# Kernel optimization log

Measured on AMD Instinct MI355X. Metric: run time of the kernel, lower is better.

Reference implementation:

```python
import jax, jax.numpy as jnp
import numpy as np

B, C, H, W = 2, 256, 128, 128
S = 256          # num superpixels
QK = 256         # qk_dim
NUM_HEADS = 8
TOPK = 128
SCALE = (QK // NUM_HEADS) ** -0.5
EPS = 1e-5


def setup_inputs() -> dict:
    key = jax.random.key(0)
    k0, k1, k2, k3, k4 = jax.random.split(key, 5)
    x = jax.random.normal(k0, (B, C, H, W), jnp.float32)
    affinity_matrix = jax.random.normal(k1, (B, S, H * W), jnp.float32)
    wq = jax.random.normal(k2, (QK, C), jnp.float32) * 0.05
    wk = jax.random.normal(k3, (QK, C), jnp.float32) * 0.05
    wv = jax.random.normal(k4, (C, C), jnp.float32) * 0.05
    return {
        "x": x,
        "affinity_matrix": affinity_matrix,
        "ln_weight": jnp.ones((C,), jnp.float32),
        "ln_bias": jnp.zeros((C,), jnp.float32),
        "wq": wq,
        "wk": wk,
        "wv": wv,
        "num_spixels": S,
    }


def _forward(x, affinity_matrix, ln_weight, ln_bias, wq, wk, wv, num_spixels):
    Bx, Cx, Hx, Wx = x.shape
    HW = Hx * Wx
    h = NUM_HEADS
    T = TOPK
    Sx = num_spixels

    # LayerNorm2d: normalize over channel dim per pixel
    mu = x.mean(axis=1, keepdims=True)
    var = ((x - mu) ** 2).mean(axis=1, keepdims=True)
    xn = (x - mu) * jax.lax.rsqrt(var + EPS)
    xn = xn * ln_weight[None, :, None, None] + ln_bias[None, :, None, None]
    xf = xn.reshape(Bx, Cx, HW)

    # 1x1 convs as GEMMs: [out_ch, in_ch] x [B, in_ch, HW]
    q = jnp.einsum('oc,bcn->bon', wq, xf)   # [B, QK, HW]
    k = jnp.einsum('oc,bcn->bon', wk, xf)   # [B, QK, HW]
    v = jnp.einsum('oc,bcn->bon', wv, xf)   # [B, C,  HW]

    # top-k pixels per superpixel
    sims, indices = jax.lax.top_k(affinity_matrix, T)  # [B, S, T]

    def gath(t):  # t [B, D, HW] -> [B, D, S, T]
        return jax.vmap(lambda tb, ib: tb[:, ib])(t, indices)

    def heads(t):  # [B, D, S, T] -> [B, S, h, T, D//h]
        D = t.shape[1]
        return t.reshape(Bx, h, D // h, Sx, T).transpose(0, 3, 1, 4, 2)

    qh = heads(gath(q))  # [B,S,h,T,cq]
    kh = heads(gath(k))
    vh = heads(gath(v))  # [B,S,h,T,cv]

    attn = jnp.einsum('bshtc,bshuc->bshtu', qh, kh) * SCALE
    attn = jax.nn.softmax(attn, axis=-1)

    w = sims[:, :, None, :, None]            # [B,S,1,T,1]
    vw = vh * w                               # kweight=True
    out = jnp.einsum('bshtu,bshuc->bshtc', attn, vw)

    # 'b k h t c -> b (h c) (k t)'
    out = out.transpose(0, 2, 4, 1, 3).reshape(Bx, Cx, Sx * T)
    out = out * sims.reshape(Bx, 1, Sx * T)  # weight is broadcast over channels

    idx = indices.reshape(Bx, Sx * T)
    # weighted_scatter_mean with normz=False: tgt is v itself (not zeros)
    res = jax.vmap(lambda vb, ib, sb: vb.at[:, ib].add(sb))(v, idx, out)
    return res.reshape(Bx, Cx, Hx, Wx)


def reference(x, affinity_matrix, ln_weight, ln_bias, wq, wk, wv, num_spixels):
    return _forward(x, affinity_matrix, ln_weight, ln_bias, wq, wk, wv, num_spixels)
```

## Files before the change

### kernel.cpp

```cpp
#include <hip/hip_runtime.h>

#define HW      16384
#define C_DIM   256
#define S_DIM   256
#define T_K     128
#define NH      8
#define DH      32
#define QKV_ST  768
#define B_DIM   2
#define SCALE_F 0.17677669529663687f
#define CAND    1536
#define EQCAP   512
#define NROWS   (S_DIM * T_K)

typedef __attribute__((ext_vector_type(8))) short short8;
typedef __attribute__((ext_vector_type(4))) float f32x4;
typedef __attribute__((ext_vector_type(4))) unsigned uint4v;

__device__ __forceinline__ short f2bf(float f) {
    union { __bf16 h; short s; } u;
    u.h = (__bf16)f;
    return u.s;
}
__device__ __forceinline__ float bf2f(short s) {
    unsigned u = ((unsigned)(unsigned short)s) << 16;
    return __uint_as_float(u);
}

__device__ __forceinline__ unsigned sortkey(float f) {
    unsigned u = __float_as_uint(f);
    return (u & 0x80000000u) ? ~u : (u | 0x80000000u);
}
__device__ __forceinline__ float keyval(unsigned k) {
    return __uint_as_float((k & 0x80000000u) ? (k ^ 0x80000000u) : ~k);
}

__launch_bounds__(256)
__global__ void ln_fused_kernel(const float* __restrict__ x,
                                const float* __restrict__ g,
                                const float* __restrict__ beta,
                                short* __restrict__ xnT) {
    int b  = blockIdx.y;
    int n0 = blockIdx.x * 64;
    int tid = threadIdx.x;

    __shared__ float t[256][67];
    __shared__ float ps[4][64], pss[4][64];
    __shared__ float mu_s[64], rs_s[64];

    {
        int cl = tid >> 2;
        int ni = (tid & 3) * 16;
#pragma unroll
        for (int gset = 0; gset < 4; gset++) {
            int c = cl + gset * 64;
            const float* src = x + ((size_t)b * C_DIM + c) * HW + n0 + ni;
#pragma unroll
            for (int j = 0; j < 4; j++) {
                float4 v = *(const float4*)(src + j * 4);
                t[c][ni + j * 4 + 0] = v.x;
                t[c][ni + j * 4 + 1] = v.y;
                t[c][ni + j * 4 + 2] = v.z;
                t[c][ni + j * 4 + 3] = v.w;
            }
        }
    }
    __syncthreads();

    {
        int q = tid >> 6;
        int l = tid & 63;
        float s = 0.f, ss = 0.f;
#pragma unroll
        for (int c = 0; c < 64; c++) {
            float v = t[q * 64 + c][l];
            s += v; ss += v * v;
        }
        ps[q][l] = s; pss[q][l] = ss;
    }
    __syncthreads();
    if (tid < 64) {
        float S  = ps[0][tid] + ps[1][tid] + ps[2][tid] + ps[3][tid];
        float SS = pss[0][tid] + pss[1][tid] + pss[2][tid] + pss[3][tid];
        float m   = S * (1.f / C_DIM);
        float var = fmaxf(SS * (1.f / C_DIM) - m * m, 0.f);
        mu_s[tid] = m;
        rs_s[tid] = rsqrtf(var + 1e-5f);
    }
    __syncthreads();

    {
        int nl  = tid >> 2;
        int ci0 = (tid & 3) * 16;
        float m  = mu_s[nl];
        float rs = rs_s[nl];
        short* dst = xnT + ((size_t)b * HW + n0 + nl) * C_DIM;
#pragma unroll
        for (int gset = 0; gset < 4; gset++) {
            int ci = ci0 + gset * 64;
            short8 s0, s1;
#pragma unroll
            for (int j = 0; j < 8; j++) {
                int c = ci + j;
                s0[j] = f2bf((t[c][nl] - m) * rs * g[c] + beta[c]);
            }
#pragma unroll
            for (int j = 0; j < 8; j++) {
                int c = ci + 8 + j;
                s1[j] = f2bf((t[c][nl] - m) * rs * g[c] + beta[c]);
            }
            *(short8*)(dst + ci)     = s0;
            *(short8*)(dst + ci + 8) = s1;
        }
    }
}

__global__ void wpack_kernel(const float* __restrict__ wq,
                             const float* __restrict__ wk,
                             const float* __restrict__ wv,
                             short* __restrict__ wb) {
    int gid  = blockIdx.x * 256 + threadIdx.x;
    int base = gid * 4;
    int o = base >> 8;
    int c = base & 255;
    const float* src = (o < 256) ? wq + (size_t)o * 256
                     : (o < 512) ? wk + (size_t)(o - 256) * 256
                                 : wv + (size_t)(o - 512) * 256;
    float4 w4 = *(const float4*)(src + c);
    short4 s4;
    s4.x = f2bf(w4.x); s4.y = f2bf(w4.y); s4.z = f2bf(w4.z); s4.w = f2bf(w4.w);
    *(short4*)&wb[base] = s4;
}

#define E_STRIDE 136
#define A_STR   36
__launch_bounds__(256)
__global__ void qkv_mfma_kernel(const short* __restrict__ xnT,
                                const short* __restrict__ wb,
                                short* __restrict__ qkv) {
    int b  = blockIdx.z;
    int n0 = blockIdx.x * 128;
    int o0 = blockIdx.y * 128;
    int tid  = threadIdx.x;
    int wv   = tid >> 6;
    int wn   = wv & 1;
    int wo   = wv >> 1;
    int lane = tid & 63;
    int quad = lane >> 4;
    int ln   = lane & 15;

    __shared__ __align__(16) union {
        short S[2][128 * A_STR];
        short Es[64 * E_STRIDE];
    } L;

    int r1 = tid >> 2,        q1 = tid & 3;
    int r2 = (tid + 256) >> 2, q2 = (tid + 256) & 3;
    const short* gA1 = xnT + ((size_t)b * HW + n0 + r1) * C_DIM + q1 * 8;
    const short* gA2 = xnT + ((size_t)b * HW + n0 + r2) * C_DIM + q2 * 8;
    const short* gB1 = wb + (size_t)(o0 + r1) * C_DIM + q1 * 8;
    const short* gB2 = wb + (size_t)(o0 + r2) * C_DIM + q2 * 8;
    int la1 = r1 * A_STR + q1 * 8;
    int la2 = r2 * A_STR + q2 * 8;

    int aoff[4], boff[4];
#pragma unroll
    for (int mt = 0; mt < 4; mt++)
        aoff[mt] = (wn * 64 + mt * 16 + ln) * A_STR + quad * 8;
#pragma unroll
    for (int nt = 0; nt < 4; nt++)
        boff[nt] = (wo * 64 + nt * 16 + ln) * A_STR + quad * 8;

    f32x4 acc[4][4];
    const f32x4 zero4 = {0.f, 0.f, 0.f, 0.f};
#pragma unroll
    for (int mt = 0; mt < 4; mt++)
#pragma unroll
        for (int nt = 0; nt < 4; nt++) acc[mt][nt] = zero4;

    {
        short8 ra1 = *(const short8*)gA1;
        short8 ra2 = *(const short8*)gA2;
        short8 rb1 = *(const short8*)gB1;
        short8 rb2 = *(const short8*)gB2;
        *(short8*)&L.S[0][la1] = ra1;
        *(short8*)&L.S[0][la2] = ra2;
        *(short8*)&L.S[1][la1] = rb1;
        *(short8*)&L.S[1][la2] = rb2;
    }
    __syncthreads();

    for (int t = 0; t < 8; t++) {
        short8 ra1, ra2, rb1, rb2;
        if (t < 7) {
            int c0 = (t + 1) * 32;
            ra1 = *(const short8*)(gA1 + c0);
            ra2 = *(const short8*)(gA2 + c0);
            rb1 = *(const short8*)(gB1 + c0);
            rb2 = *(const short8*)(gB2 + c0);
        }

        short8 af[4], bf[4];
#pragma unroll
        for (int mt = 0; mt < 4; mt++) af[mt] = *(const short8*)&L.S[0][aoff[mt]];
#pragma unroll
        for (int nt = 0; nt < 4; nt++) bf[nt] = *(const short8*)&L.S[1][boff[nt]];
        __builtin_amdgcn_s_setprio(1);
#pragma unroll
        for (int mt = 0; mt < 4; mt++)
#pragma unroll
            for (int nt = 0; nt < 4; nt++)
                acc[mt][nt] = __builtin_amdgcn_mfma_f32_16x16x32_bf16(af[mt], bf[nt], acc[mt][nt], 0, 0, 0);
        __builtin_amdgcn_s_setprio(0);

        __syncthreads();
        if (t < 7) {
            *(short8*)&L.S[0][la1] = ra1;
            *(short8*)&L.S[0][la2] = ra2;
            *(short8*)&L.S[1][la1] = rb1;
            *(short8*)&L.S[1][la2] = rb2;
            __syncthreads();
        }
    }

#pragma unroll
    for (int p = 0; p < 2; p++) {
        if (wn == p) {
#pragma unroll
            for (int mt = 0; mt < 4; mt++)
#pragma unroll
                for (int nt = 0; nt < 4; nt++)
#pragma unroll
                    for (int r = 0; r < 4; r++)
                        L.Es[(mt * 16 + quad * 4 + r) * E_STRIDE + wo * 64 + nt * 16 + ln] =
                            f2bf(acc[mt][nt][r]);
        }
        __syncthreads();
        {
            int nl = tid >> 2;
            int qo = (tid & 3) * 32;
            const short* srcr = &L.Es[nl * E_STRIDE + qo];
            short* dst = qkv + ((size_t)b * HW + n0 + p * 64 + nl) * QKV_ST + o0 + qo;
#pragma unroll
            for (int j = 0; j < 4; j++)
                *(short8*)(dst + j * 8) = *(const short8*)(srcr + j * 8);
        }
        __syncthreads();
    }
}

__launch_bounds__(1024)
__global__ void topk_kernel(const float* __restrict__ aff,
                            float* __restrict__ sims,
                            int* __restrict__ idx,
                            int* __restrict__ cnt) {
    int s = blockIdx.x, b = blockIdx.y;
    int tid = threadIdx.x;
    const float4* rowv4 = (const float4*)(aff + ((size_t)b * S_DIM + s) * HW);
    int* cntb = cnt + b * HW;

    __shared__ union {
        unsigned rowk[HW];
        unsigned short eqix_u[EQCAP];
    } U;
    __shared__ unsigned hist[256];
    __shared__ unsigned sufs[256];
    __shared__ unsigned ckey[CAND];
    __shared__ unsigned short cidx[CAND];
    __shared__ int s_sel, cHi, cCand, cEq;

    if (tid == 0) { cHi = 0; cCand = 0; cEq = 0; }
    if (tid < 256) hist[tid] = 0;
    __syncthreads();

    for (int i = tid; i < HW / 4; i += 1024) {
        float4 v = rowv4[i];
        uint4v k;
        k[0] = sortkey(v.x); k[1] = sortkey(v.y);
        k[2] = sortkey(v.z); k[3] = sortkey(v.w);
        *(uint4v*)&U.rowk[i * 4] = k;
        atomicAdd(&hist[k[0] >> 24], 1u);
        atomicAdd(&hist[k[1] >> 24], 1u);
        atomicAdd(&hist[k[2] >> 24], 1u);
        atomicAdd(&hist[k[3] >> 24], 1u);
    }
    __syncthreads();

    if (tid < 256) sufs[tid] = hist[tid];
    __syncthreads();
#pragma unroll
    for (int off = 1; off < 256; off <<= 1) {
        unsigned v = 0;
        if (tid < 256 && tid + off < 256) v = sufs[tid + off];
        __syncthreads();
        if (tid < 256) sufs[tid] += v;
        __syncthreads();
    }

    int kneed = T_K;
    if (tid < 256) {
        unsigned above = (tid < 255) ? sufs[tid + 1] : 0u;
        if ((int)sufs[tid] >= kneed && (int)above < kneed) s_sel = tid;
    }
    __syncthreads();
    int sel = s_sel;
    unsigned prefix = (unsigned)sel << 24;
    kneed -= (int)((sel < 255) ? sufs[sel + 1] : 0u);
    __syncthreads();

    float* so = sims + ((size_t)b * S_DIM + s) * T_K;
    int*   io = idx  + ((size_t)b * S_DIM + s) * T_K;

    for (int i = tid; i < HW; i += 1024) {
        unsigned u  = U.rowk[i];
        unsigned hb = u >> 24;
        if (hb > (unsigned)sel) {
            int p = atomicAdd(&cHi, 1);
            so[p] = keyval(u); io[p] = i;
            atomicAdd(&cntb[i], 1);
        } else if (hb == (unsigned)sel) {
            int c = atomicAdd(&cCand, 1);
            if (c < CAND) { ckey[c] = u; cidx[c] = (unsigned short)i; }
        }
    }
    __syncthreads();
    int nc = min(cCand, CAND);

    for (int shift = 16; shift >= 0; shift -= 8) {
        if (tid < 256) hist[tid] = 0;
        __syncthreads();
        unsigned mask = 0xFFFFFFFFu << (shift + 8);
        for (int i = tid; i < nc; i += 1024) {
            unsigned u = ckey[i];
            if ((u & mask) == prefix) atomicAdd(&hist[(u >> shift) & 255], 1u);
        }
        __syncthreads();
        if (tid < 256) sufs[tid] = hist[tid];
        __syncthreads();
#pragma unroll
        for (int off = 1; off < 256; off <<= 1) {
            unsigned v = 0;
            if (tid < 256 && tid + off < 256) v = sufs[tid + off];
            __syncthreads();
            if (tid < 256) sufs[tid] += v;
            __syncthreads();
        }
        if (tid < 256) {
            unsigned above = (tid < 255) ? sufs[tid + 1] : 0u;
            if ((int)sufs[tid] >= kneed && (int)above < kneed) s_sel = tid;
        }
        __syncthreads();
        sel = s_sel;
        prefix |= (unsigned)sel << shift;
        kneed  -= (int)((sel < 255) ? sufs[sel + 1] : 0u);
        __syncthreads();
    }

    unsigned T = prefix;
    int kneedF = kneed;
    __syncthreads();

    for (int i = tid; i < nc; i += 1024) {
        unsigned u = ckey[i];
        if (u > T) {
            int p = atomicAdd(&cHi, 1);
            so[p] = keyval(u); io[p] = cidx[i];
            atomicAdd(&cntb[cidx[i]], 1);
        } else if (u == T) {
            int q = atomicAdd(&cEq, 1);
            if (q < EQCAP) U.eqix_u[q] = cidx[i];
        }
    }
    __syncthreads();
    int m = min(cEq, EQCAP);

    float tval = keyval(T);
    for (int i = tid; i < m; i += 1024) {
        int my = U.eqix_u[i];
        int rank = 0;
        for (int j = 0; j < m; j++) rank += (U.eqix_u[j] < my);
        if (rank < kneedF) {
            so[127 - rank] = tval; io[127 - rank] = my;
            atomicAdd(&cntb[my], 1);
        }
    }
}

__launch_bounds__(1024)
__global__ void scan_kernel(const int* __restrict__ cnt,
                            int* __restrict__ offs) {
    int b = blockIdx.x;
    const int* c = cnt + b * HW;
    int* o = offs + b * HW;
    int tid = threadIdx.x;
    __shared__ int part[1024];
    int base = tid * 16;
    int loc[16];
    int s = 0;
#pragma unroll
    for (int j = 0; j < 16; j++) { loc[j] = s; s += c[base + j]; }
    part[tid] = s;
    __syncthreads();
    for (int off = 1; off < 1024; off <<= 1) {
        int v = (tid >= off) ? part[tid - off] : 0;
        __syncthreads();
        part[tid] += v;
        __syncthreads();
    }
    int pre = (tid == 0) ? 0 : part[tid - 1];
#pragma unroll
    for (int j = 0; j < 16; j++) o[base + j] = pre + loc[j];
}

__global__ void fill_kernel(const int* __restrict__ idx,
                            const int* __restrict__ offs,
                            int* __restrict__ fcnt,
                            int* __restrict__ slots) {
    int b = blockIdx.y;
    int i = blockIdx.x * 256 + threadIdx.x;
    int n = idx[(size_t)b * NROWS + i];
    int r = atomicAdd(&fcnt[b * HW + n], 1);
    slots[(size_t)b * NROWS + offs[b * HW + n] + r] = i;
}

#define K_STRIDE 40
#define VT_STRIDE 132
union KPu {
    short K[T_K * K_STRIDE];
    short P[4][16 * VT_STRIDE];
};
__launch_bounds__(256)
__global__ void attn_kernel(const short* __restrict__ qkv,
                            const float* __restrict__ sims,
                            const int* __restrict__ idx,
                            float* __restrict__ dout) {
    int s = blockIdx.x, h = blockIdx.y, b = blockIdx.z;
    int tid  = threadIdx.x;
    int wv   = tid >> 6;
    int lane = tid & 63;
    int quad = lane >> 4;
    int ln   = lane & 15;

    __shared__ __align__(16) KPu KP;
    __shared__ __align__(16) short Vt[DH * VT_STRIDE];
    __shared__ float sim_s[T_K];
    __shared__ int   idx_s[T_K];

    if (tid < T_K) {
        sim_s[tid] = sims[((size_t)b * S_DIM + s) * T_K + tid];
        idx_s[tid] = idx [((size_t)b * S_DIM + s) * T_K + tid];
    }
    __syncthreads();

    const short* qkvb = qkv + (size_t)b * HW * QKV_ST;
    int co = h * DH;

    {
        int r  = tid >> 1;
        int hh = tid & 1;
        const short* base = qkvb + (size_t)idx_s[r] * QKV_ST + co + hh * 16;
        short8 k0 = *(const short8*)(base + 256);
        short8 k1 = *(const short8*)(base + 256 + 8);
        *(short8*)&KP.K[r * K_STRIDE + hh * 16]     = k0;
        *(short8*)&KP.K[r * K_STRIDE + hh * 16 + 8] = k1;
        float suR = sim_s[r];
        short8 v0 = *(const short8*)(base + 512);
        short8 v1 = *(const short8*)(base + 512 + 8);
#pragma unroll
        for (int i = 0; i < 8; i++)
            Vt[(hh * 16 + i) * VT_STRIDE + r]     = f2bf(bf2f(v0[i]) * suR);
#pragma unroll
        for (int i = 0; i < 8; i++)
            Vt[(hh * 16 + 8 + i) * VT_STRIDE + r] = f2bf(bf2f(v1[i]) * suR);
    }

    short8 aq[2];
#pragma unroll
    for (int mt = 0; mt < 2; mt++) {
        int t = wv * 32 + mt * 16 + ln;
        aq[mt] = *(const short8*)(qkvb + (size_t)idx_s[t] * QKV_ST + co + quad * 8);
    }
    __syncthreads();

    f32x4 S[2][8];
    const f32x4 zero4 = {0.f, 0.f, 0.f, 0.f};
    __builtin_amdgcn_s_setprio(1);
#pragma unroll
    for (int nt = 0; nt < 8; nt++) {
        short8 kf = *(const short8*)&KP.K[(nt * 16 + ln) * K_STRIDE + quad * 8];
        S[0][nt] = __builtin_amdgcn_mfma_f32_16x16x32_bf16(aq[0], kf, zero4, 0, 0, 0);
        S[1][nt] = __builtin_amdgcn_mfma_f32_16x16x32_bf16(aq[1], kf, zero4, 0, 0, 0);
    }
    __builtin_amdgcn_s_setprio(0);

    float lrow[2][4];
#pragma unroll
    for (int mt = 0; mt < 2; mt++) {
#pragma unroll
        for (int r = 0; r < 4; r++) {
            float l = 0.f;
#pragma unroll
            for (int nt = 0; nt < 8; nt++) {
                float p = __expf(S[mt][nt][r] * SCALE_F);
                S[mt][nt][r] = p;
                l += p;
            }
            l += __shfl_xor(l, 1, 64);
            l += __shfl_xor(l, 2, 64);
            l += __shfl_xor(l, 4, 64);
            l += __shfl_xor(l, 8, 64);
            lrow[mt][r] = l;
        }
    }

    __syncthreads();

    float* db = dout + ((size_t)b * NROWS + s * T_K) * C_DIM + co;
#pragma unroll
    for (int mt = 0; mt < 2; mt++) {
        float w[4];
#pragma unroll
        for (int r = 0; r < 4; r++)
            w[r] = sim_s[wv * 32 + mt * 16 + quad * 4 + r] / lrow[mt][r];

#pragma unroll
        for (int nt = 0; nt < 8; nt++) {
#pragma unroll
            for (int r = 0; r < 4; r++)
                KP.P[wv][(quad * 4 + r) * VT_STRIDE + nt * 16 + ln] = f2bf(S[mt][nt][r]);
        }

        f32x4 O[2] = {zero4, zero4};
        __builtin_amdgcn_s_setprio(1);
#pragma unroll
        for (int kt = 0; kt < 4; kt++) {
            short8 pa = *(const short8*)&KP.P[wv][ln * VT_STRIDE + kt * 32 + quad * 8];
#pragma unroll
            for (int nt2 = 0; nt2 < 2; nt2++) {
                short8 vb = *(const short8*)&Vt[(nt2 * 16 + ln) * VT_STRIDE + kt * 32 + quad * 8];
                O[nt2] = __builtin_amdgcn_mfma_f32_16x16x32_bf16(pa, vb, O[nt2], 0, 0, 0);
            }
        }
        __builtin_amdgcn_s_setprio(0);

#pragma unroll
        for (int nt2 = 0; nt2 < 2; nt2++)
#pragma unroll
            for (int r = 0; r < 4; r++) {
                int t = wv * 32 + mt * 16 + quad * 4 + r;
                db[(size_t)t * C_DIM + nt2 * 16 + ln] = O[nt2][r] * w[r];
            }
    }
}

__launch_bounds__(256)
__global__ void transpose_add_kernel(const short* __restrict__ qkv,
                                     const float* __restrict__ dout,
                                     const int* __restrict__ cnt,
                                     const int* __restrict__ offs,
                                     const int* __restrict__ slots,
                                     float* __restrict__ out) {
    int b  = blockIdx.z;
    int n0 = blockIdx.x * 32;
    int c0 = blockIdx.y * 128;
    int x4 = threadIdx.x & 31;
    int y  = threadIdx.x >> 5;

    const float* doutb = dout + (size_t)b * NROWS * C_DIM;
    const int*   slb   = slots + (size_t)b * NROWS;

    __shared__ float t[32][129];

#pragma unroll
    for (int r = 0; r < 4; r++) {
        int px = y + 8 * r;
        int n  = n0 + px;
        size_t row = (size_t)b * HW + n;
        short4 vs = *(const short4*)(qkv + row * QKV_ST + 512 + c0 + x4 * 4);
        float a0 = bf2f(vs.x), a1 = bf2f(vs.y), a2 = bf2f(vs.z), a3 = bf2f(vs.w);
        int cn = cnt[b * HW + n];
        int of = offs[b * HW + n];
        for (int j = 0; j < cn; j++) {
            int dr = slb[of + j];
            float4 d = *(const float4*)(doutb + (size_t)dr * C_DIM + c0 + x4 * 4);
            a0 += d.x; a1 += d.y; a2 += d.z; a3 += d.w;
        }
        t[px][x4 * 4 + 0] = a0;
        t[px][x4 * 4 + 1] = a1;
        t[px][x4 * 4 + 2] = a2;
        t[px][x4 * 4 + 3] = a3;
    }
    __syncthreads();

    {
        int nl = threadIdx.x & 31;
        int cg = threadIdx.x >> 5;
#pragma unroll
        for (int cc = 0; cc < 16; cc++) {
            int c = c0 + cg * 16 + cc;
            out[((size_t)b * C_DIM + c) * HW + n0 + nl] = t[nl][cg * 16 + cc];
        }
    }
}

extern "C" void kernel_launch(void* const* d_in, const int* in_sizes, int n_in,
                              void* d_out, int out_size, void* d_ws, size_t ws_size,
                              hipStream_t stream) {
    const float* x    = (const float*)d_in[0];
    const float* aff  = (const float*)d_in[1];
    const float* g    = (const float*)d_in[2];
    const float* beta = (const float*)d_in[3];
    const float* wq   = (const float*)d_in[4];
    const float* wk   = (const float*)d_in[5];
    const float* wv   = (const float*)d_in[6];
    float* out = (float*)d_out;

    char* ws = (char*)d_ws;
    short* qkv  = (short*)ws;                                   ws += (size_t)B_DIM * HW * QKV_ST * 2;
    short* xnT  = (short*)ws;                                   ws += (size_t)B_DIM * HW * C_DIM * 2;
    short* wbuf = (short*)ws;                                   ws += (size_t)QKV_ST * C_DIM * 2;
    float* simsb= (float*)ws;                                   ws += (size_t)B_DIM * S_DIM * T_K * 4;
    int*   idxb = (int*)ws;                                     ws += (size_t)B_DIM * S_DIM * T_K * 4;
    int*   cntb = (int*)ws;                                     ws += (size_t)B_DIM * HW * 4;
    int*   offsb= (int*)ws;                                     ws += (size_t)B_DIM * HW * 4;
    int*   fcnt = (int*)ws;                                     ws += (size_t)B_DIM * HW * 4;
    int*   slots= (int*)ws;                                     ws += (size_t)B_DIM * NROWS * 4;
    float* dout = (float*)ws;

    hipMemsetAsync(cntb, 0, (size_t)B_DIM * HW * sizeof(int), stream);
    hipMemsetAsync(fcnt, 0, (size_t)B_DIM * HW * sizeof(int), stream);

    ln_fused_kernel<<<dim3(HW / 64, B_DIM), 256, 0, stream>>>(x, g, beta, xnT);
    wpack_kernel<<<dim3(QKV_ST * C_DIM / 4 / 256), 256, 0, stream>>>(wq, wk, wv, wbuf);
    qkv_mfma_kernel<<<dim3(HW / 128, QKV_ST / 128, B_DIM), 256, 0, stream>>>(
        xnT, wbuf, qkv);
    topk_kernel<<<dim3(S_DIM, B_DIM), 1024, 0, stream>>>(aff, simsb, idxb, cntb);
    scan_kernel<<<dim3(B_DIM), 1024, 0, stream>>>(cntb, offsb);
    fill_kernel<<<dim3(NROWS / 256, B_DIM), 256, 0, stream>>>(idxb, offsb, fcnt, slots);
    attn_kernel<<<dim3(S_DIM, NH, B_DIM), 256, 0, stream>>>(qkv, simsb, idxb, dout);
    transpose_add_kernel<<<dim3(HW / 32, C_DIM / 128, B_DIM), 256, 0, stream>>>(
        qkv, dout, cntb, offsb, slots, out);
}
```

Before: 246.3 us.

## Fuse weight packing and count zeroing into LN; merge scan and fill kernels

Weight bf16 packing now runs in an extra grid row of the LayerNorm kernel, which also zeroes the per-pixel count buffer, so both memsets and the separate wpack launch go away. The scan and fill kernels are merged into one, with fill using shared-memory atomics on a copy of the offsets instead of a global counter array. This cuts launch and memset overhead. The cost is that fill now runs in only two blocks, one per batch, which serialises 32K scatter writes per block.

```diff
diff --git a/kernel.cpp b/kernel.cpp
--- a/kernel.cpp
+++ b/kernel.cpp
@@ -12,6 +12,7 @@
 #define CAND    1536
 #define EQCAP   512
 #define NROWS   (S_DIM * T_K)
+#define WPACK_BLOCKS (QKV_ST * C_DIM / 4 / 256)
 
 typedef __attribute__((ext_vector_type(8))) short short8;
 typedef __attribute__((ext_vector_type(4))) float f32x4;
@@ -39,10 +40,35 @@
 __global__ void ln_fused_kernel(const float* __restrict__ x,
                                 const float* __restrict__ g,
                                 const float* __restrict__ beta,
-                                short* __restrict__ xnT) {
+                                short* __restrict__ xnT,
+                                const float* __restrict__ wq,
+                                const float* __restrict__ wk,
+                                const float* __restrict__ wv,
+                                short* __restrict__ wb,
+                                int* __restrict__ cnt) {
+    int tid = threadIdx.x;
+
+    if (blockIdx.y == B_DIM) {
+        if (blockIdx.x < WPACK_BLOCKS) {
+            int gid  = blockIdx.x * 256 + tid;
+            int base = gid * 4;
+            int o = base >> 8;
+            int c = base & 255;
+            const float* src = (o < 256) ? wq + (size_t)o * 256
+                             : (o < 512) ? wk + (size_t)(o - 256) * 256
+                                         : wv + (size_t)(o - 512) * 256;
+            float4 w4 = *(const float4*)(src + c);
+            short4 s4;
+            s4.x = f2bf(w4.x); s4.y = f2bf(w4.y); s4.z = f2bf(w4.z); s4.w = f2bf(w4.w);
+            *(short4*)&wb[base] = s4;
+        }
+        return;
+    }
+
     int b  = blockIdx.y;
     int n0 = blockIdx.x * 64;
-    int tid = threadIdx.x;
+
+    if (tid < 64) cnt[b * HW + n0 + tid] = 0;
 
     __shared__ float t[256][67];
     __shared__ float ps[4][64], pss[4][64];
@@ -113,23 +139,6 @@
             *(short8*)(dst + ci + 8) = s1;
         }
     }
-}
-
-__global__ void wpack_kernel(const float* __restrict__ wq,
-                             const float* __restrict__ wk,
-                             const float* __restrict__ wv,
-                             short* __restrict__ wb) {
-    int gid  = blockIdx.x * 256 + threadIdx.x;
-    int base = gid * 4;
-    int o = base >> 8;
-    int c = base & 255;
-    const float* src = (o < 256) ? wq + (size_t)o * 256
-                     : (o < 512) ? wk + (size_t)(o - 256) * 256
-                                 : wv + (size_t)(o - 512) * 256;
-    float4 w4 = *(const float4*)(src + c);
-    short4 s4;
-    s4.x = f2bf(w4.x); s4.y = f2bf(w4.y); s4.z = f2bf(w4.z); s4.w = f2bf(w4.w);
-    *(short4*)&wb[base] = s4;
 }
 
 #define E_STRIDE 136
@@ -387,13 +396,18 @@
 }
 
 __launch_bounds__(1024)
-__global__ void scan_kernel(const int* __restrict__ cnt,
-                            int* __restrict__ offs) {
+__global__ void scan_fill_kernel(const int* __restrict__ cnt,
+                                 const int* __restrict__ idx,
+                                 int* __restrict__ offs,
+                                 int* __restrict__ slots) {
     int b = blockIdx.x;
     const int* c = cnt + b * HW;
     int* o = offs + b * HW;
     int tid = threadIdx.x;
+
     __shared__ int part[1024];
+    __shared__ int fcntL[HW];
+
     int base = tid * 16;
     int loc[16];
     int s = 0;
@@ -409,18 +423,20 @@
     }
     int pre = (tid == 0) ? 0 : part[tid - 1];
 #pragma unroll
-    for (int j = 0; j < 16; j++) o[base + j] = pre + loc[j];
-}
-
-__global__ void fill_kernel(const int* __restrict__ idx,
-                            const int* __restrict__ offs,
-                            int* __restrict__ fcnt,
-                            int* __restrict__ slots) {
-    int b = blockIdx.y;
-    int i = blockIdx.x * 256 + threadIdx.x;
-    int n = idx[(size_t)b * NROWS + i];
-    int r = atomicAdd(&fcnt[b * HW + n], 1);
-    slots[(size_t)b * NROWS + offs[b * HW + n] + r] = i;
+    for (int j = 0; j < 16; j++) {
+        int ov = pre + loc[j];
+        o[base + j]     = ov;
+        fcntL[base + j] = ov;
+    }
+    __syncthreads();
+
+    const int* ib = idx + (size_t)b * NROWS;
+    int* sb = slots + (size_t)b * NROWS;
+    for (int i = tid; i < NROWS; i += 1024) {
+        int n = ib[i];
+        int slot = atomicAdd(&fcntL[n], 1);
+        sb[slot] = i;
+    }
 }
 
 #define K_STRIDE 40
@@ -623,20 +639,15 @@
     int*   idxb = (int*)ws;                                     ws += (size_t)B_DIM * S_DIM * T_K * 4;
     int*   cntb = (int*)ws;                                     ws += (size_t)B_DIM * HW * 4;
     int*   offsb= (int*)ws;                                     ws += (size_t)B_DIM * HW * 4;
-    int*   fcnt = (int*)ws;                                     ws += (size_t)B_DIM * HW * 4;
     int*   slots= (int*)ws;                                     ws += (size_t)B_DIM * NROWS * 4;
     float* dout = (float*)ws;
 
-    hipMemsetAsync(cntb, 0, (size_t)B_DIM * HW * sizeof(int), stream);
-    hipMemsetAsync(fcnt, 0, (size_t)B_DIM * HW * sizeof(int), stream);
-
-    ln_fused_kernel<<<dim3(HW / 64, B_DIM), 256, 0, stream>>>(x, g, beta, xnT);
-    wpack_kernel<<<dim3(QKV_ST * C_DIM / 4 / 256), 256, 0, stream>>>(wq, wk, wv, wbuf);
+    ln_fused_kernel<<<dim3(HW / 64, B_DIM + 1), 256, 0, stream>>>(
+        x, g, beta, xnT, wq, wk, wv, wbuf, cntb);
     qkv_mfma_kernel<<<dim3(HW / 128, QKV_ST / 128, B_DIM), 256, 0, stream>>>(
         xnT, wbuf, qkv);
     topk_kernel<<<dim3(S_DIM, B_DIM), 1024, 0, stream>>>(aff, simsb, idxb, cntb);
-    scan_kernel<<<dim3(B_DIM), 1024, 0, stream>>>(cntb, offsb);
-    fill_kernel<<<dim3(NROWS / 256, B_DIM), 256, 0, stream>>>(idxb, offsb, fcnt, slots);
+    scan_fill_kernel<<<dim3(B_DIM), 1024, 0, stream>>>(cntb, idxb, offsb, slots);
     attn_kernel<<<dim3(S_DIM, NH, B_DIM), 256, 0, stream>>>(qkv, simsb, idxb, dout);
     transpose_add_kernel<<<dim3(HW / 32, C_DIM / 128, B_DIM), 256, 0, stream>>>(
         qkv, dout, cntb, offsb, slots, out);
```

Result: slower. 265.7 us (+7.9%).
